# Kernel tuning notes

Measured on AMD Instinct MI355X. Metric: run time of the kernel, lower is better.

The kernel has to match this reference:

```python
import jax, jax.numpy as jnp
import numpy as np

MARGIN = 1.0
EPS = 1e-7  # added to the difference vector, matching F.pairwise_distance


def setup_inputs() -> dict:
    key = jax.random.key(0)
    k1, k2, k3 = jax.random.split(key, 3)
    B, D = 8192, 512
    feats = jax.random.normal(k1, (B, D), dtype=jnp.float32)
    labels = jax.random.randint(k2, (B,), 0, 2).astype(jnp.int64)
    # noise[0] drives positive sampling, noise[1] drives negative sampling
    noise = jax.random.uniform(k3, (2, B, B), dtype=jnp.float32)
    return {"feats": feats, "labels": labels, "noise": noise}


def reference(feats, labels, noise):
    # feats: [B, D], labels: [B] in {0,1}, noise: [2, B, B]
    pos_mask = labels[None, :] == labels[:, None]        # [B, B] same-label
    neg_mask = labels[None, :] == (1 - labels)[:, None]  # [B, B] opposite-label

    # Uniform sample among matching indices via argmax of masked iid uniforms.
    pos_idx = jnp.argmax(jnp.where(pos_mask, noise[0], -1.0), axis=1)  # [B]
    neg_idx = jnp.argmax(jnp.where(neg_mask, noise[1], -1.0), axis=1)  # [B]

    # Positive set always contains the anchor itself (count >= 1).
    positive = feats[pos_idx]                                           # [B, D]
    # If no negatives exist, the original falls back to the anchor feat.
    has_neg = neg_mask.any(axis=1)                                      # [B]
    negative = jnp.where(has_neg[:, None], feats[neg_idx], feats)       # [B, D]

    # TripletMarginLoss(margin=1, p=2, eps=1e-7), reduction='mean'
    d_ap = jnp.linalg.norm(feats - positive + EPS, axis=1)
    d_an = jnp.linalg.norm(feats - negative + EPS, axis=1)
    return jnp.mean(jax.nn.relu(d_ap - d_an + MARGIN))
```

## Files before the change

### kernel.cpp

```cpp
#include <hip/hip_runtime.h>

constexpr int Bn = 8192;
constexpr int Dn = 512;
#define EPSF 1e-7f
#define MARGINF 1.0f

__device__ __forceinline__ void amax_combine(float& bv, int& bi, float v, int i) {
    if (v > bv || (v == bv && i < bi)) { bv = v; bi = i; }
}

__global__ __launch_bounds__(256) void pack_labels_kernel(const int* __restrict__ labels,
                                                          unsigned* __restrict__ packed) {
    __shared__ int s_any;
    const int tid = threadIdx.x;
    if (tid == 0) s_any = 0;
    __syncthreads();
    if (tid < 128 && labels[2 * tid + 1] != 0) atomicOr(&s_any, 1);
    __syncthreads();
    const bool is64 = (s_any == 0);

    if (is64) {
        const long long* l8 = (const long long*)labels;
        for (int w = tid; w < Bn / 4; w += 256) {
            unsigned b0 = (unsigned)l8[w * 4 + 0] & 0xffu;
            unsigned b1 = (unsigned)l8[w * 4 + 1] & 0xffu;
            unsigned b2 = (unsigned)l8[w * 4 + 2] & 0xffu;
            unsigned b3 = (unsigned)l8[w * 4 + 3] & 0xffu;
            packed[w] = b0 | (b1 << 8) | (b2 << 16) | (b3 << 24);
        }
    } else {
        for (int w = tid; w < Bn / 4; w += 256) {
            int4 v = ((const int4*)labels)[w];
            packed[w] = ((unsigned)v.x & 0xffu) | (((unsigned)v.y & 0xffu) << 8) |
                        (((unsigned)v.z & 0xffu) << 16) | (((unsigned)v.w & 0xffu) << 24);
        }
    }
}

__global__ __launch_bounds__(256) void triplet_main(
    const float*    __restrict__ feats,
    const unsigned* __restrict__ packed,
    const float*    __restrict__ noise,
    float*          __restrict__ losses)
{
    __shared__ unsigned slab_u[Bn / 4];
    __shared__ float swv[8];
    __shared__ int   swi[8];
    __shared__ float sdist[8];
    __shared__ int   sidx[2];

    const int row  = blockIdx.x;
    const int tid  = threadIdx.x;
    const int lane = tid & 63;
    const int wv   = tid >> 6;

    for (int k = tid; k < Bn / 16; k += 256)
        ((uint4*)slab_u)[k] = ((const uint4*)packed)[k];
    __syncthreads();

    const unsigned myLab = (slab_u[row >> 2] >> ((row & 3) * 8)) & 0xffu;

    float pbv[4] = {-1.0f, -1.0f, -1.0f, -1.0f};
    float nbv[4] = {-1.0f, -1.0f, -1.0f, -1.0f};
    int   pbi[4] = {0x7FFFFFFF, 0x7FFFFFFF, 0x7FFFFFFF, 0x7FFFFFFF};
    int   nbi[4] = {0x7FFFFFFF, 0x7FFFFFFF, 0x7FFFFFFF, 0x7FFFFFFF};

    const float* __restrict__ n0 = noise + (size_t)row * Bn;
    const float* __restrict__ n1 = noise + (size_t)Bn * Bn + (size_t)row * Bn;

    for (int j = tid * 4; j < Bn; j += 256 * 4) {
        float4 v0 = *(const float4*)(n0 + j);
        float4 v1 = *(const float4*)(n1 + j);
        unsigned lw = slab_u[j >> 2];
        const float* f0 = (const float*)&v0;
        const float* f1 = (const float*)&v1;
#pragma unroll
        for (int k = 0; k < 4; ++k) {
            unsigned lk = (lw >> (k * 8)) & 0xffu;
            float cp = (lk == myLab) ? f0[k] : -1.0f;
            if (cp > pbv[k]) { pbv[k] = cp; pbi[k] = j + k; }
            float cn = (lk != myLab) ? f1[k] : -1.0f;
            if (cn > nbv[k]) { nbv[k] = cn; nbi[k] = j + k; }
        }
    }

    float pv = pbv[0]; int pi_ = pbi[0];
    float nv = nbv[0]; int ni_ = nbi[0];
#pragma unroll
    for (int k = 1; k < 4; ++k) {
        amax_combine(pv, pi_, pbv[k], pbi[k]);
        amax_combine(nv, ni_, nbv[k], nbi[k]);
    }

    for (int off = 32; off; off >>= 1) {
        float ov = __shfl_down(pv, off, 64);
        int   oi = __shfl_down(pi_, off, 64);
        amax_combine(pv, pi_, ov, oi);
        ov = __shfl_down(nv, off, 64);
        oi = __shfl_down(ni_, off, 64);
        amax_combine(nv, ni_, ov, oi);
    }
    if (lane == 0) { swv[wv] = pv; swi[wv] = pi_; swv[wv + 4] = nv; swi[wv + 4] = ni_; }
    __syncthreads();

    if (tid == 0) {
        float bv = swv[0]; int bi = swi[0];
        for (int k = 1; k < 4; ++k) amax_combine(bv, bi, swv[k], swi[k]);
        float bv2 = swv[4]; int bi2 = swi[4];
        for (int k = 5; k < 8; ++k) amax_combine(bv2, bi2, swv[k], swi[k]);
        sidx[0] = bi;
        sidx[1] = (bv2 >= 0.0f) ? bi2 : row;
    }
    __syncthreads();

    const int pi = sidx[0];
    const int ni = sidx[1];

    const float2 a  = ((const float2*)(feats + (size_t)row * Dn))[tid];
    const float2 p  = ((const float2*)(feats + (size_t)pi  * Dn))[tid];
    const float2 nn = ((const float2*)(feats + (size_t)ni  * Dn))[tid];

    float dx = a.x - p.x + EPSF, dy = a.y - p.y + EPSF;
    float dap = dx * dx + dy * dy;
    dx = a.x - nn.x + EPSF; dy = a.y - nn.y + EPSF;
    float dan = dx * dx + dy * dy;

    for (int off = 32; off; off >>= 1) {
        dap += __shfl_down(dap, off, 64);
        dan += __shfl_down(dan, off, 64);
    }
    if (lane == 0) { sdist[wv] = dap; sdist[wv + 4] = dan; }
    __syncthreads();

    if (tid == 0) {
        float sap = sdist[0] + sdist[1] + sdist[2] + sdist[3];
        float san = sdist[4] + sdist[5] + sdist[6] + sdist[7];
        losses[row] = fmaxf(sqrtf(sap) - sqrtf(san) + MARGINF, 0.0f);
    }
}

__global__ __launch_bounds__(256) void reduce_mean_kernel(
    const float* __restrict__ losses, float* __restrict__ out)
{
    const int tid  = threadIdx.x;
    const int lane = tid & 63;
    const int wv   = tid >> 6;
    float s = 0.0f;
    for (int k = tid; k < Bn; k += 256) s += losses[k];
    for (int off = 32; off; off >>= 1) s += __shfl_down(s, off, 64);
    __shared__ float sw[4];
    if (lane == 0) sw[wv] = s;
    __syncthreads();
    if (tid == 0) out[0] = (sw[0] + sw[1] + sw[2] + sw[3]) * (1.0f / (float)Bn);
}

extern "C" void kernel_launch(void* const* d_in, const int* in_sizes, int n_in,
                              void* d_out, int out_size, void* d_ws, size_t ws_size,
                              hipStream_t stream) {
    const float* feats  = (const float*)d_in[0];
    const int*   labels = (const int*)d_in[1];
    const float* noise  = (const float*)d_in[2];
    float* out = (float*)d_out;

    float*    losses = (float*)d_ws;
    unsigned* packed = (unsigned*)((char*)d_ws + 32768);

    pack_labels_kernel<<<1, 256, 0, stream>>>(labels, packed);
    triplet_main<<<Bn, 256, 0, stream>>>(feats, packed, noise, losses);
    reduce_mean_kernel<<<1, 256, 0, stream>>>(losses, out);
}
```

Baseline: 113.2 us.

## Fuse label packing, per-row triplet loss, and mean into one wave-per-row kernel

Merges the three kernels into one. Each block packs the labels into shared memory itself, and each of its four waves handles one row's argmax scan and distance. This removes the block-level shuffles and syncs per row. The mean is computed with fixed-point 64-bit atomics and a last-block-done counter, which adds a memset launch. In exchange, every block repeats the label-pack work and the loss gets quantized at a 2^-24 scale.

```diff
diff --git a/kernel.cpp b/kernel.cpp
--- a/kernel.cpp
+++ b/kernel.cpp
@@ -2,17 +2,30 @@
 
 constexpr int Bn = 8192;
 constexpr int Dn = 512;
+constexpr int ROWS_PER_BLOCK = 4;
 #define EPSF 1e-7f
 #define MARGINF 1.0f
+#define FPSCALE 16777216.0
 
 __device__ __forceinline__ void amax_combine(float& bv, int& bi, float v, int i) {
     if (v > bv || (v == bv && i < bi)) { bv = v; bi = i; }
 }
 
-__global__ __launch_bounds__(256) void pack_labels_kernel(const int* __restrict__ labels,
-                                                          unsigned* __restrict__ packed) {
+__global__ __launch_bounds__(256) void triplet_fused(
+    const float* __restrict__ feats,
+    const int*   __restrict__ labels,
+    const float* __restrict__ noise,
+    unsigned long long* __restrict__ ws,
+    float*       __restrict__ out)
+{
+    __shared__ unsigned slab_u[Bn / 4];
     __shared__ int s_any;
-    const int tid = threadIdx.x;
+    __shared__ unsigned long long s_q[ROWS_PER_BLOCK];
+
+    const int tid  = threadIdx.x;
+    const int lane = tid & 63;
+    const int wv   = tid >> 6;
+
     if (tid == 0) s_any = 0;
     __syncthreads();
     if (tid < 128 && labels[2 * tid + 1] != 0) atomicOr(&s_any, 1);
@@ -26,49 +39,30 @@
             unsigned b1 = (unsigned)l8[w * 4 + 1] & 0xffu;
             unsigned b2 = (unsigned)l8[w * 4 + 2] & 0xffu;
             unsigned b3 = (unsigned)l8[w * 4 + 3] & 0xffu;
-            packed[w] = b0 | (b1 << 8) | (b2 << 16) | (b3 << 24);
+            slab_u[w] = b0 | (b1 << 8) | (b2 << 16) | (b3 << 24);
         }
     } else {
         for (int w = tid; w < Bn / 4; w += 256) {
             int4 v = ((const int4*)labels)[w];
-            packed[w] = ((unsigned)v.x & 0xffu) | (((unsigned)v.y & 0xffu) << 8) |
+            slab_u[w] = ((unsigned)v.x & 0xffu) | (((unsigned)v.y & 0xffu) << 8) |
                         (((unsigned)v.z & 0xffu) << 16) | (((unsigned)v.w & 0xffu) << 24);
         }
     }
-}
-
-__global__ __launch_bounds__(256) void triplet_main(
-    const float*    __restrict__ feats,
-    const unsigned* __restrict__ packed,
-    const float*    __restrict__ noise,
-    float*          __restrict__ losses)
-{
-    __shared__ unsigned slab_u[Bn / 4];
-    __shared__ float swv[8];
-    __shared__ int   swi[8];
-    __shared__ float sdist[8];
-    __shared__ int   sidx[2];
-
-    const int row  = blockIdx.x;
-    const int tid  = threadIdx.x;
-    const int lane = tid & 63;
-    const int wv   = tid >> 6;
-
-    for (int k = tid; k < Bn / 16; k += 256)
-        ((uint4*)slab_u)[k] = ((const uint4*)packed)[k];
     __syncthreads();
 
+    const int row = blockIdx.x * ROWS_PER_BLOCK + wv;
     const unsigned myLab = (slab_u[row >> 2] >> ((row & 3) * 8)) & 0xffu;
+
+    const float* __restrict__ n0 = noise + (size_t)row * Bn;
+    const float* __restrict__ n1 = noise + (size_t)Bn * Bn + (size_t)row * Bn;
 
     float pbv[4] = {-1.0f, -1.0f, -1.0f, -1.0f};
     float nbv[4] = {-1.0f, -1.0f, -1.0f, -1.0f};
     int   pbi[4] = {0x7FFFFFFF, 0x7FFFFFFF, 0x7FFFFFFF, 0x7FFFFFFF};
     int   nbi[4] = {0x7FFFFFFF, 0x7FFFFFFF, 0x7FFFFFFF, 0x7FFFFFFF};
 
-    const float* __restrict__ n0 = noise + (size_t)row * Bn;
-    const float* __restrict__ n1 = noise + (size_t)Bn * Bn + (size_t)row * Bn;
-
-    for (int j = tid * 4; j < Bn; j += 256 * 4) {
+#pragma unroll 2
+    for (int j = lane * 4; j < Bn; j += 256) {
         float4 v0 = *(const float4*)(n0 + j);
         float4 v1 = *(const float4*)(n1 + j);
         unsigned lw = slab_u[j >> 2];
@@ -100,58 +94,52 @@
         oi = __shfl_down(ni_, off, 64);
         amax_combine(nv, ni_, ov, oi);
     }
-    if (lane == 0) { swv[wv] = pv; swi[wv] = pi_; swv[wv + 4] = nv; swi[wv + 4] = ni_; }
-    __syncthreads();
+    const int   pi  = __shfl(pi_, 0, 64);
+    int         ni  = __shfl(ni_, 0, 64);
+    const float nvb = __shfl(nv, 0, 64);
+    if (nvb < 0.0f) ni = row;
 
-    if (tid == 0) {
-        float bv = swv[0]; int bi = swi[0];
-        for (int k = 1; k < 4; ++k) amax_combine(bv, bi, swv[k], swi[k]);
-        float bv2 = swv[4]; int bi2 = swi[4];
-        for (int k = 5; k < 8; ++k) amax_combine(bv2, bi2, swv[k], swi[k]);
-        sidx[0] = bi;
-        sidx[1] = (bv2 >= 0.0f) ? bi2 : row;
+    const float* fa = feats + (size_t)row * Dn;
+    const float* fp = feats + (size_t)pi  * Dn;
+    const float* fn = feats + (size_t)ni  * Dn;
+    float dap = 0.0f, dan = 0.0f;
+#pragma unroll
+    for (int c = 0; c < 2; ++c) {
+        const int o = c * 256 + lane * 4;
+        float4 a = *(const float4*)(fa + o);
+        float4 p = *(const float4*)(fp + o);
+        float4 q = *(const float4*)(fn + o);
+        float d;
+        d = a.x - p.x + EPSF; dap += d * d;
+        d = a.y - p.y + EPSF; dap += d * d;
+        d = a.z - p.z + EPSF; dap += d * d;
+        d = a.w - p.w + EPSF; dap += d * d;
+        d = a.x - q.x + EPSF; dan += d * d;
+        d = a.y - q.y + EPSF; dan += d * d;
+        d = a.z - q.z + EPSF; dan += d * d;
+        d = a.w - q.w + EPSF; dan += d * d;
     }
-    __syncthreads();
-
-    const int pi = sidx[0];
-    const int ni = sidx[1];
-
-    const float2 a  = ((const float2*)(feats + (size_t)row * Dn))[tid];
-    const float2 p  = ((const float2*)(feats + (size_t)pi  * Dn))[tid];
-    const float2 nn = ((const float2*)(feats + (size_t)ni  * Dn))[tid];
-
-    float dx = a.x - p.x + EPSF, dy = a.y - p.y + EPSF;
-    float dap = dx * dx + dy * dy;
-    dx = a.x - nn.x + EPSF; dy = a.y - nn.y + EPSF;
-    float dan = dx * dx + dy * dy;
-
     for (int off = 32; off; off >>= 1) {
         dap += __shfl_down(dap, off, 64);
         dan += __shfl_down(dan, off, 64);
     }
-    if (lane == 0) { sdist[wv] = dap; sdist[wv + 4] = dan; }
+    if (lane == 0) {
+        float loss = fmaxf(sqrtf(dap) - sqrtf(dan) + MARGINF, 0.0f);
+        s_q[wv] = (unsigned long long)llrint((double)loss * FPSCALE);
+    }
     __syncthreads();
 
     if (tid == 0) {
-        float sap = sdist[0] + sdist[1] + sdist[2] + sdist[3];
-        float san = sdist[4] + sdist[5] + sdist[6] + sdist[7];
-        losses[row] = fmaxf(sqrtf(sap) - sqrtf(san) + MARGINF, 0.0f);
+        unsigned long long q = s_q[0] + s_q[1] + s_q[2] + s_q[3];
+        atomicAdd(ws, q);
+        __threadfence();
+        unsigned done = atomicAdd((unsigned*)(ws + 1), 1u);
+        if (done == gridDim.x - 1) {
+            __threadfence();
+            unsigned long long s = atomicAdd(ws, 0ULL);
+            out[0] = (float)((double)s / FPSCALE / (double)Bn);
+        }
     }
-}
-
-__global__ __launch_bounds__(256) void reduce_mean_kernel(
-    const float* __restrict__ losses, float* __restrict__ out)
-{
-    const int tid  = threadIdx.x;
-    const int lane = tid & 63;
-    const int wv   = tid >> 6;
-    float s = 0.0f;
-    for (int k = tid; k < Bn; k += 256) s += losses[k];
-    for (int off = 32; off; off >>= 1) s += __shfl_down(s, off, 64);
-    __shared__ float sw[4];
-    if (lane == 0) sw[wv] = s;
-    __syncthreads();
-    if (tid == 0) out[0] = (sw[0] + sw[1] + sw[2] + sw[3]) * (1.0f / (float)Bn);
 }
 
 extern "C" void kernel_launch(void* const* d_in, const int* in_sizes, int n_in,
@@ -160,12 +148,8 @@
     const float* feats  = (const float*)d_in[0];
     const int*   labels = (const int*)d_in[1];
     const float* noise  = (const float*)d_in[2];
-    float* out = (float*)d_out;
 
-    float*    losses = (float*)d_ws;
-    unsigned* packed = (unsigned*)((char*)d_ws + 32768);
-
-    pack_labels_kernel<<<1, 256, 0, stream>>>(labels, packed);
-    triplet_main<<<Bn, 256, 0, stream>>>(feats, packed, noise, losses);
-    reduce_mean_kernel<<<1, 256, 0, stream>>>(losses, out);
+    hipMemsetAsync(d_ws, 0, 16, stream);
+    triplet_fused<<<Bn / ROWS_PER_BLOCK, 256, 0, stream>>>(
+        feats, labels, noise, (unsigned long long*)d_ws, (float*)d_out);
 }
```

Result: slower. 203.5 us (+79.7%).
